# Kernel optimization log

Hardware: AMD Instinct MI355X
Metric: run time of the kernel (lower is better)

The kernel has to match this reference:

```python
import jax, jax.numpy as jnp
import numpy as np

NEG = -1e6  # mask value used by d2l-style masked_softmax


def masked_softmax(scores, valid_lens):
    # scores: [B, Q, K]; valid_lens: [B] int — mask key positions j >= valid_len
    K = scores.shape[-1]
    mask = jnp.arange(K, dtype=jnp.int32)[None, None, :] < valid_lens[:, None, None]
    scores = jnp.where(mask, scores, NEG)
    return jax.nn.softmax(scores, axis=-1)


def setup_inputs() -> dict:
    key = jax.random.key(0)
    kq, kk, kv, kl = jax.random.split(key, 4)
    B, Q, K, d = 16, 4096, 4096, 128
    queries = jax.random.normal(kq, (B, Q, d), dtype=jnp.float32)
    keys = jax.random.normal(kk, (B, K, d), dtype=jnp.float32)
    values = jax.random.normal(kv, (B, K, d), dtype=jnp.float32)
    valid_lens = jax.random.randint(kl, (B,), 1, K + 1, dtype=jnp.int32)
    return {"queries": queries, "keys": keys, "values": values,
            "valid_lens": valid_lens}


def reference(queries, keys, values, valid_lens):
    d = queries.shape[-1]
    # [B, Q, K] scores = Q K^T / sqrt(d)
    scores = jnp.einsum('bqd,bkd->bqk', queries, keys) / jnp.sqrt(
        jnp.asarray(d, queries.dtype))
    attn = masked_softmax(scores, valid_lens)
    # dropout is identity in eval mode
    return jnp.einsum('bqk,bkd->bqd', attn, values)
```

## Files before the change

### kernel.cpp

```cpp
#include <hip/hip_runtime.h>
#include <stdint.h>

typedef __attribute__((ext_vector_type(8))) short short8;
typedef __attribute__((ext_vector_type(4))) float float4v;

#define B_  16
#define S_  4096
#define D_  128
#define TM  64
#define TN  64
#define NT_ (S_ / TN)
#define IMG 8192

__device__ __forceinline__ unsigned short f2bf(float f) {
    union { float f; uint32_t u; } c; c.f = f;
    uint32_t u = c.u + 0x7FFFu + ((c.u >> 16) & 1u);
    return (unsigned short)(u >> 16);
}

__device__ __forceinline__ uint4 pack8(float4v x, float4v y) {
    uint4 r;
    r.x = (uint32_t)f2bf(x[0]) | ((uint32_t)f2bf(x[1]) << 16);
    r.y = (uint32_t)f2bf(x[2]) | ((uint32_t)f2bf(x[3]) << 16);
    r.z = (uint32_t)f2bf(y[0]) | ((uint32_t)f2bf(y[1]) << 16);
    r.w = (uint32_t)f2bf(y[2]) | ((uint32_t)f2bf(y[3]) << 16);
    return r;
}

__device__ __forceinline__ void gload16(const unsigned short* g, unsigned short* l) {
    __builtin_amdgcn_global_load_lds(
        (const __attribute__((address_space(1))) unsigned int*)g,
        (__attribute__((address_space(3))) unsigned int*)l, 16, 0, 0);
}

__global__ __launch_bounds__(256)
void prepass(const float* __restrict__ Kg, const float* __restrict__ Vg,
             unsigned short* __restrict__ Kb, unsigned short* __restrict__ Vb)
{
    const int t = threadIdx.x;
    const int tile = blockIdx.x, b = blockIdx.y;
    const size_t img = (size_t)(b * NT_ + tile) * IMG;

    const float* ksrc = Kg + ((size_t)b * S_ + tile * TN) * D_;
    const float* vsrc = Vg + ((size_t)b * S_ + tile * TN) * D_;
    unsigned short* kdst = Kb + img;
    unsigned short* vdst = Vb + img;

    float4v kx[4], ky[4];
    #pragma unroll
    for (int i = 0; i < 4; ++i) {
        int bid = i * 256 + t;
        int row = bid >> 4, cbp = bid & 15;
        int cb  = cbp ^ (row & 7);
        const float* s = ksrc + row * D_ + cb * 8;
        kx[i] = *(const float4v*)s;
        ky[i] = *(const float4v*)(s + 4);
    }
    const int kb = t >> 5, cg = t & 31;
    float4v v[8];
    #pragma unroll
    for (int r = 0; r < 8; ++r)
        v[r] = *(const float4v*)(vsrc + (kb * 8 + r) * D_ + cg * 4);

    #pragma unroll
    for (int i = 0; i < 4; ++i) {
        int bid = i * 256 + t;
        *(uint4*)(kdst + (size_t)bid * 8) = pack8(kx[i], ky[i]);
    }

    #pragma unroll
    for (int j = 0; j < 4; ++j) {
        int dr = cg * 4 + j;
        uint4 w;
        w.x = (uint32_t)f2bf(v[0][j]) | ((uint32_t)f2bf(v[1][j]) << 16);
        w.y = (uint32_t)f2bf(v[2][j]) | ((uint32_t)f2bf(v[3][j]) << 16);
        w.z = (uint32_t)f2bf(v[4][j]) | ((uint32_t)f2bf(v[5][j]) << 16);
        w.w = (uint32_t)f2bf(v[6][j]) | ((uint32_t)f2bf(v[7][j]) << 16);
        *(uint4*)(vdst + dr * 64 + (kb ^ (dr & 7)) * 8) = w;
    }
}

__global__ __launch_bounds__(256, 4)
void attn_fwd(const float* __restrict__ Qg,
              const unsigned short* __restrict__ Kb,
              const unsigned short* __restrict__ Vb,
              const int* __restrict__ VL,
              float* __restrict__ Og)
{
    __shared__ __align__(16) unsigned short Ks[TN * D_];
    __shared__ __align__(16) unsigned short Vt[D_ * TN];
    __shared__ __align__(16) unsigned short Ps[4 * 16 * 64];

    const int t    = threadIdx.x;
    const int wave = t >> 6;
    const int lane = t & 63;
    const int l16  = lane & 15;
    const int quad = lane >> 4;
    const int sw   = l16 & 7;

    const int b  = blockIdx.y;
    const int q0 = blockIdx.x * TM;
    const int nvalid = VL[b];
    const int ntiles = (nvalid + TN - 1) / TN;

    const float scale = 0.08838834764831845f;

    short8 qf[4];
    {
        const float* qp = Qg + ((size_t)b * S_ + (q0 + wave * 16 + l16)) * D_;
        #pragma unroll
        for (int ks = 0; ks < 4; ++ks) {
            float4v x = *(const float4v*)(qp + ks * 32 + quad * 8);
            float4v y = *(const float4v*)(qp + ks * 32 + quad * 8 + 4);
            #pragma unroll
            for (int j = 0; j < 4; ++j) { x[j] *= scale; y[j] *= scale; }
            union { uint4 u; short8 s; } cv; cv.u = pack8(x, y);
            qf[ks] = cv.s;
        }
    }

    float4v oacc[8];
    #pragma unroll
    for (int dt = 0; dt < 8; ++dt) oacc[dt] = (float4v){0.f, 0.f, 0.f, 0.f};
    float lsum[4] = {0.f, 0.f, 0.f, 0.f};

    unsigned short* Pw = Ps + wave * (16 * 64);

    for (int tile = 0; tile < ntiles; ++tile) {
        const int n0 = tile * TN;
        __syncthreads();

        {
            const unsigned short* kimg = Kb + (size_t)(b * NT_ + tile) * IMG;
            const unsigned short* vimg = Vb + (size_t)(b * NT_ + tile) * IMG;
            #pragma unroll
            for (int i = 0; i < 4; ++i) {
                int go = (i * 256 + t) * 8;
                int lo = (i * 256 + wave * 64) * 8;
                gload16(kimg + go, &Ks[lo]);
                gload16(vimg + go, &Vt[lo]);
            }
        }
        __syncthreads();

        float sv[4][4];
        #pragma unroll
        for (int nt = 0; nt < 4; ++nt) {
            float4v sa = (float4v){0.f, 0.f, 0.f, 0.f};
            #pragma unroll
            for (int ks = 0; ks < 4; ++ks) {
                short8 bf = *(const short8*)(&Ks[(nt * 16 + l16) * D_ + (((ks << 2) + quad) ^ sw) * 8]);
                sa = __builtin_amdgcn_mfma_f32_16x16x32_bf16(qf[ks], bf, sa, 0, 0, 0);
            }
            #pragma unroll
            for (int r = 0; r < 4; ++r) sv[nt][r] = sa[r];
        }

        const bool full = (n0 + TN) <= nvalid;
        #pragma unroll
        for (int nt = 0; nt < 4; ++nt) {
            const bool ok = full || (n0 + nt * 16 + l16) < nvalid;
            const int cb = nt * 2 + (l16 >> 3);
            #pragma unroll
            for (int r = 0; r < 4; ++r) {
                float p = ok ? __expf(sv[nt][r]) : 0.0f;
                lsum[r] += p;
                const int row = quad * 4 + r;
                Pw[row * 64 + ((cb ^ (row >> 1)) << 3) + sw] = f2bf(p);
            }
        }

        #pragma unroll
        for (int ks2 = 0; ks2 < 2; ++ks2) {
            short8 pf = *(const short8*)(&Pw[l16 * 64 + ((((ks2 << 2) + quad) ^ (l16 >> 1)) << 3)]);
            #pragma unroll
            for (int dt = 0; dt < 8; ++dt) {
                short8 vf = *(const short8*)(&Vt[(dt * 16 + l16) * TN + ((((ks2 << 2) + quad) ^ sw) << 3)]);
                oacc[dt] = __builtin_amdgcn_mfma_f32_16x16x32_bf16(pf, vf, oacc[dt], 0, 0, 0);
            }
        }
    }

    float invl[4];
    #pragma unroll
    for (int r = 0; r < 4; ++r) {
        float s = lsum[r];
        #pragma unroll
        for (int off = 1; off < 16; off <<= 1)
            s += __shfl_xor(s, off);
        invl[r] = 1.0f / s;
    }

    float* op = Og + ((size_t)b * S_ + (q0 + wave * 16 + quad * 4)) * D_;
    #pragma unroll
    for (int r = 0; r < 4; ++r) {
        #pragma unroll
        for (int dt = 0; dt < 8; ++dt)
            op[r * D_ + dt * 16 + l16] = oacc[dt][r] * invl[r];
    }
}

extern "C" void kernel_launch(void* const* d_in, const int* in_sizes, int n_in,
                              void* d_out, int out_size, void* d_ws, size_t ws_size,
                              hipStream_t stream) {
    const float* Q = (const float*)d_in[0];
    const float* K = (const float*)d_in[1];
    const float* V = (const float*)d_in[2];
    const int*   L = (const int*)d_in[3];
    float*       O = (float*)d_out;

    unsigned short* Kb = (unsigned short*)d_ws;
    unsigned short* Vb = Kb + (size_t)B_ * S_ * D_;

    dim3 grid(NT_, B_);
    prepass<<<grid, 256, 0, stream>>>(K, V, Kb, Vb);
    dim3 grid2(S_ / TM, B_);
    attn_fwd<<<grid2, 256, 0, stream>>>(Q, Kb, Vb, L, O);
}
```

Before: 227.7 us.

## Switch attention to 32x32 MFMA with transposed S and register-resident P

```diff
diff --git a/kernel.cpp b/kernel.cpp
--- a/kernel.cpp
+++ b/kernel.cpp
@@ -3,6 +3,7 @@
 
 typedef __attribute__((ext_vector_type(8))) short short8;
 typedef __attribute__((ext_vector_type(4))) float float4v;
+typedef __attribute__((ext_vector_type(16))) float f32x16;
 
 #define B_  16
 #define S_  4096
@@ -12,6 +13,8 @@
 #define NT_ (S_ / TN)
 #define IMG 8192
 
+#define ZERO16 {0.f,0.f,0.f,0.f, 0.f,0.f,0.f,0.f, 0.f,0.f,0.f,0.f, 0.f,0.f,0.f,0.f}
+
 __device__ __forceinline__ unsigned short f2bf(float f) {
     union { float f; uint32_t u; } c; c.f = f;
     uint32_t u = c.u + 0x7FFFu + ((c.u >> 16) & 1u);
@@ -33,6 +36,24 @@
         (__attribute__((address_space(3))) unsigned int*)l, 16, 0, 0);
 }
 
+__device__ __forceinline__ uint32_t cvtpk(float lo, float hi) {
+    uint32_t w;
+    asm("v_cvt_pk_bf16_f32 %0, %1, %2" : "=v"(w) : "v"(lo), "v"(hi));
+    return w;
+}
+
+__device__ __forceinline__ short8 build_pfrag(const float* p) {
+    uint32_t xa = cvtpk(p[0], p[1]);
+    uint32_t xb = cvtpk(p[2], p[3]);
+    uint32_t ya = cvtpk(p[4], p[5]);
+    uint32_t yb = cvtpk(p[6], p[7]);
+    asm("v_permlane32_swap_b32 %0, %1" : "+v"(xa), "+v"(ya));
+    asm("v_permlane32_swap_b32 %0, %1" : "+v"(xb), "+v"(yb));
+    union { uint32_t u[4]; short8 s; } r;
+    r.u[0] = xa; r.u[1] = xb; r.u[2] = ya; r.u[3] = yb;
+    return r.s;
+}
+
 __global__ __launch_bounds__(256)
 void prepass(const float* __restrict__ Kg, const float* __restrict__ Vg,
              unsigned short* __restrict__ Kb, unsigned short* __restrict__ Vb)
@@ -51,7 +72,7 @@
     for (int i = 0; i < 4; ++i) {
         int bid = i * 256 + t;
         int row = bid >> 4, cbp = bid & 15;
-        int cb  = cbp ^ (row & 7);
+        int cb  = cbp ^ (row & 15);
         const float* s = ksrc + row * D_ + cb * 8;
         kx[i] = *(const float4v*)s;
         ky[i] = *(const float4v*)(s + 4);
@@ -80,7 +101,7 @@
     }
 }
 
-__global__ __launch_bounds__(256, 4)
+__global__ __launch_bounds__(128, 2)
 void attn_fwd(const float* __restrict__ Qg,
               const unsigned short* __restrict__ Kb,
               const unsigned short* __restrict__ Vb,
@@ -89,42 +110,41 @@
 {
     __shared__ __align__(16) unsigned short Ks[TN * D_];
     __shared__ __align__(16) unsigned short Vt[D_ * TN];
-    __shared__ __align__(16) unsigned short Ps[4 * 16 * 64];
 
     const int t    = threadIdx.x;
     const int wave = t >> 6;
     const int lane = t & 63;
-    const int l16  = lane & 15;
-    const int quad = lane >> 4;
-    const int sw   = l16 & 7;
+    const int l31  = lane & 31;
+    const int hi   = lane >> 5;
 
     const int b  = blockIdx.y;
     const int q0 = blockIdx.x * TM;
     const int nvalid = VL[b];
     const int ntiles = (nvalid + TN - 1) / TN;
 
-    const float scale = 0.08838834764831845f;
-
-    short8 qf[4];
+    const float qscale = 0.08838834764831845f * 1.4426950408889634f;
+
+    short8 qf[8];
     {
-        const float* qp = Qg + ((size_t)b * S_ + (q0 + wave * 16 + l16)) * D_;
+        const float* qp = Qg + ((size_t)b * S_ + (q0 + wave * 32 + l31)) * D_;
         #pragma unroll
-        for (int ks = 0; ks < 4; ++ks) {
-            float4v x = *(const float4v*)(qp + ks * 32 + quad * 8);
-            float4v y = *(const float4v*)(qp + ks * 32 + quad * 8 + 4);
-            #pragma unroll
-            for (int j = 0; j < 4; ++j) { x[j] *= scale; y[j] *= scale; }
+        for (int ks = 0; ks < 8; ++ks) {
+            float4v x = *(const float4v*)(qp + ks * 16 + hi * 8);
+            float4v y = *(const float4v*)(qp + ks * 16 + hi * 8 + 4);
+            #pragma unroll
+            for (int j = 0; j < 4; ++j) { x[j] *= qscale; y[j] *= qscale; }
             union { uint4 u; short8 s; } cv; cv.u = pack8(x, y);
             qf[ks] = cv.s;
         }
     }
 
-    float4v oacc[8];
-    #pragma unroll
-    for (int dt = 0; dt < 8; ++dt) oacc[dt] = (float4v){0.f, 0.f, 0.f, 0.f};
-    float lsum[4] = {0.f, 0.f, 0.f, 0.f};
-
-    unsigned short* Pw = Ps + wave * (16 * 64);
+    f32x16 zz = ZERO16;
+    f32x16 oacc[4];
+    oacc[0] = zz; oacc[1] = zz; oacc[2] = zz; oacc[3] = zz;
+    float lsum = 0.f;
+
+    const int swk = l31 & 15;
+    const int swv = l31 & 7;
 
     for (int tile = 0; tile < ntiles; ++tile) {
         const int n0 = tile * TN;
@@ -134,69 +154,85 @@
             const unsigned short* kimg = Kb + (size_t)(b * NT_ + tile) * IMG;
             const unsigned short* vimg = Vb + (size_t)(b * NT_ + tile) * IMG;
             #pragma unroll
-            for (int i = 0; i < 4; ++i) {
-                int go = (i * 256 + t) * 8;
-                int lo = (i * 256 + wave * 64) * 8;
+            for (int i = 0; i < 8; ++i) {
+                int go = (i * 128 + t) * 8;
+                int lo = (i * 128 + wave * 64) * 8;
                 gload16(kimg + go, &Ks[lo]);
                 gload16(vimg + go, &Vt[lo]);
             }
         }
         __syncthreads();
 
-        float sv[4][4];
+        f32x16 st0 = zz, st1 = zz;
+        {
+            const unsigned short* k0 = &Ks[l31 * D_];
+            const unsigned short* k1 = &Ks[(32 + l31) * D_];
+            __builtin_amdgcn_s_setprio(1);
+            #pragma unroll
+            for (int ks = 0; ks < 8; ++ks) {
+                int sl = (((ks << 1) | hi) ^ swk) << 3;
+                short8 a0 = *(const short8*)(k0 + sl);
+                short8 a1 = *(const short8*)(k1 + sl);
+                st0 = __builtin_amdgcn_mfma_f32_32x32x16_bf16(a0, qf[ks], st0, 0, 0, 0);
+                st1 = __builtin_amdgcn_mfma_f32_32x32x16_bf16(a1, qf[ks], st1, 0, 0, 0);
+            }
+            __builtin_amdgcn_s_setprio(0);
+        }
+
+        float p0[16], p1[16];
+        const bool full = (n0 + TN) <= nvalid;
+        if (full) {
+            #pragma unroll
+            for (int r = 0; r < 16; ++r) { p0[r] = exp2f(st0[r]); lsum += p0[r]; }
+            #pragma unroll
+            for (int r = 0; r < 16; ++r) { p1[r] = exp2f(st1[r]); lsum += p1[r]; }
+        } else {
+            #pragma unroll
+            for (int r = 0; r < 16; ++r) {
+                int key = n0 + (r & 3) + 8 * (r >> 2) + 4 * hi;
+                float e = exp2f(st0[r]);
+                p0[r] = (key < nvalid) ? e : 0.f; lsum += p0[r];
+            }
+            #pragma unroll
+            for (int r = 0; r < 16; ++r) {
+                int key = n0 + 32 + (r & 3) + 8 * (r >> 2) + 4 * hi;
+                float e = exp2f(st1[r]);
+                p1[r] = (key < nvalid) ? e : 0.f; lsum += p1[r];
+            }
+        }
+
+        short8 pf0 = build_pfrag(p0);
+        short8 pf1 = build_pfrag(p0 + 8);
+        short8 pf2 = build_pfrag(p1);
+        short8 pf3 = build_pfrag(p1 + 8);
+
+        __builtin_amdgcn_s_setprio(1);
         #pragma unroll
-        for (int nt = 0; nt < 4; ++nt) {
-            float4v sa = (float4v){0.f, 0.f, 0.f, 0.f};
-            #pragma unroll
-            for (int ks = 0; ks < 4; ++ks) {
-                short8 bf = *(const short8*)(&Ks[(nt * 16 + l16) * D_ + (((ks << 2) + quad) ^ sw) * 8]);
-                sa = __builtin_amdgcn_mfma_f32_16x16x32_bf16(qf[ks], bf, sa, 0, 0, 0);
-            }
-            #pragma unroll
-            for (int r = 0; r < 4; ++r) sv[nt][r] = sa[r];
-        }
-
-        const bool full = (n0 + TN) <= nvalid;
+        for (int dt = 0; dt < 4; ++dt) {
+            const unsigned short* vrow = &Vt[(dt * 32 + l31) * TN];
+            short8 v0 = *(const short8*)(vrow + ((((0 << 1) | hi) ^ swv) << 3));
+            short8 v1 = *(const short8*)(vrow + ((((1 << 1) | hi) ^ swv) << 3));
+            short8 v2 = *(const short8*)(vrow + ((((2 << 1) | hi) ^ swv) << 3));
+            short8 v3 = *(const short8*)(vrow + ((((3 << 1) | hi) ^ swv) << 3));
+            oacc[dt] = __builtin_amdgcn_mfma_f32_32x32x16_bf16(pf0, v0, oacc[dt], 0, 0, 0);
+            oacc[dt] = __builtin_amdgcn_mfma_f32_32x32x16_bf16(pf1, v1, oacc[dt], 0, 0, 0);
+            oacc[dt] = __builtin_amdgcn_mfma_f32_32x32x16_bf16(pf2, v2, oacc[dt], 0, 0, 0);
+            oacc[dt] = __builtin_amdgcn_mfma_f32_32x32x16_bf16(pf3, v3, oacc[dt], 0, 0, 0);
+        }
+        __builtin_amdgcn_s_setprio(0);
+    }
+
+    float ltot = lsum + __shfl_xor(lsum, 32);
+    float inv  = 1.0f / ltot;
+
+    float* op = Og + ((size_t)b * S_ + (q0 + wave * 32)) * D_ + l31;
+    #pragma unroll
+    for (int r = 0; r < 16; ++r) {
+        const int qc = (r & 3) + 8 * (r >> 2);
+        float invr = __shfl(inv, qc + 4 * hi, 32);
         #pragma unroll
-        for (int nt = 0; nt < 4; ++nt) {
-            const bool ok = full || (n0 + nt * 16 + l16) < nvalid;
-            const int cb = nt * 2 + (l16 >> 3);
-            #pragma unroll
-            for (int r = 0; r < 4; ++r) {
-                float p = ok ? __expf(sv[nt][r]) : 0.0f;
-                lsum[r] += p;
-                const int row = quad * 4 + r;
-                Pw[row * 64 + ((cb ^ (row >> 1)) << 3) + sw] = f2bf(p);
-            }
-        }
-
-        #pragma unroll
-        for (int ks2 = 0; ks2 < 2; ++ks2) {
-            short8 pf = *(const short8*)(&Pw[l16 * 64 + ((((ks2 << 2) + quad) ^ (l16 >> 1)) << 3)]);
-            #pragma unroll
-            for (int dt = 0; dt < 8; ++dt) {
-                short8 vf = *(const short8*)(&Vt[(dt * 16 + l16) * TN + ((((ks2 << 2) + quad) ^ sw) << 3)]);
-                oacc[dt] = __builtin_amdgcn_mfma_f32_16x16x32_bf16(pf, vf, oacc[dt], 0, 0, 0);
-            }
-        }
-    }
-
-    float invl[4];
-    #pragma unroll
-    for (int r = 0; r < 4; ++r) {
-        float s = lsum[r];
-        #pragma unroll
-        for (int off = 1; off < 16; off <<= 1)
-            s += __shfl_xor(s, off);
-        invl[r] = 1.0f / s;
-    }
-
-    float* op = Og + ((size_t)b * S_ + (q0 + wave * 16 + quad * 4)) * D_;
-    #pragma unroll
-    for (int r = 0; r < 4; ++r) {
-        #pragma unroll
-        for (int dt = 0; dt < 8; ++dt)
-            op[r * D_ + dt * 16 + l16] = oacc[dt][r] * invl[r];
+        for (int dt = 0; dt < 4; ++dt)
+            op[(qc + 4 * hi) * D_ + dt * 32] = oacc[dt][r] * invr;
     }
 }
 
@@ -215,5 +251,5 @@
     dim3 grid(NT_, B_);
     prepass<<<grid, 256, 0, stream>>>(K, V, Kb, Vb);
     dim3 grid2(S_ / TM, B_);
-    attn_fwd<<<grid2, 256, 0, stream>>>(Q, Kb, Vb, L, O);
-}
+    attn_fwd<<<grid2, 128, 0, stream>>>(Q, Kb, Vb, L, O);
+}
```

New measurement: 240.2 us. 5.5% more time.

## Overlap next K/V tile loads with compute using split waitcnt barriers

Applied to the files above, without the earlier changes.

```diff
diff --git a/kernel.cpp b/kernel.cpp
--- a/kernel.cpp
+++ b/kernel.cpp
@@ -51,7 +51,7 @@
     for (int i = 0; i < 4; ++i) {
         int bid = i * 256 + t;
         int row = bid >> 4, cbp = bid & 15;
-        int cb  = cbp ^ (row & 7);
+        int cb  = cbp ^ (row & 15);
         const float* s = ksrc + row * D_ + cb * 8;
         kx[i] = *(const float4v*)s;
         ky[i] = *(const float4v*)(s + 4);
@@ -96,13 +96,16 @@
     const int lane = t & 63;
     const int l16  = lane & 15;
     const int quad = lane >> 4;
-    const int sw   = l16 & 7;
+    const int swv  = l16 & 7;
 
     const int b  = blockIdx.y;
     const int q0 = blockIdx.x * TM;
     const int nvalid = VL[b];
     const int ntiles = (nvalid + TN - 1) / TN;
 
+    const unsigned short* kbase = Kb + (size_t)b * NT_ * IMG;
+    const unsigned short* vbase = Vb + (size_t)b * NT_ * IMG;
+
     const float scale = 0.08838834764831845f;
 
     short8 qf[4];
@@ -126,22 +129,19 @@
 
     unsigned short* Pw = Ps + wave * (16 * 64);
 
+    #pragma unroll
+    for (int i = 0; i < 4; ++i)
+        gload16(kbase + (i * 256 + t) * 8, &Ks[(i * 256 + wave * 64) * 8]);
+    #pragma unroll
+    for (int i = 0; i < 4; ++i)
+        gload16(vbase + (i * 256 + t) * 8, &Vt[(i * 256 + wave * 64) * 8]);
+
     for (int tile = 0; tile < ntiles; ++tile) {
         const int n0 = tile * TN;
-        __syncthreads();
-
-        {
-            const unsigned short* kimg = Kb + (size_t)(b * NT_ + tile) * IMG;
-            const unsigned short* vimg = Vb + (size_t)(b * NT_ + tile) * IMG;
-            #pragma unroll
-            for (int i = 0; i < 4; ++i) {
-                int go = (i * 256 + t) * 8;
-                int lo = (i * 256 + wave * 64) * 8;
-                gload16(kimg + go, &Ks[lo]);
-                gload16(vimg + go, &Vt[lo]);
-            }
-        }
-        __syncthreads();
+        const int nx = (tile + 1 < ntiles) ? tile + 1 : tile;
+
+        asm volatile("s_waitcnt vmcnt(4)" ::: "memory");
+        __builtin_amdgcn_s_barrier();
 
         float sv[4][4];
         #pragma unroll
@@ -149,11 +149,21 @@
             float4v sa = (float4v){0.f, 0.f, 0.f, 0.f};
             #pragma unroll
             for (int ks = 0; ks < 4; ++ks) {
-                short8 bf = *(const short8*)(&Ks[(nt * 16 + l16) * D_ + (((ks << 2) + quad) ^ sw) * 8]);
+                short8 bf = *(const short8*)(&Ks[(nt * 16 + l16) * D_ + ((((ks << 2) + quad) ^ l16) << 3)]);
                 sa = __builtin_amdgcn_mfma_f32_16x16x32_bf16(qf[ks], bf, sa, 0, 0, 0);
             }
             #pragma unroll
             for (int r = 0; r < 4; ++r) sv[nt][r] = sa[r];
+        }
+
+        asm volatile("s_waitcnt lgkmcnt(0)" ::: "memory");
+        __builtin_amdgcn_s_barrier();
+
+        {
+            const unsigned short* kimg = kbase + (size_t)nx * IMG;
+            #pragma unroll
+            for (int i = 0; i < 4; ++i)
+                gload16(kimg + (i * 256 + t) * 8, &Ks[(i * 256 + wave * 64) * 8]);
         }
 
         const bool full = (n0 + TN) <= nvalid;
@@ -166,20 +176,35 @@
                 float p = ok ? __expf(sv[nt][r]) : 0.0f;
                 lsum[r] += p;
                 const int row = quad * 4 + r;
-                Pw[row * 64 + ((cb ^ (row >> 1)) << 3) + sw] = f2bf(p);
+                Pw[row * 64 + ((cb ^ (row >> 1)) << 3) + swv] = f2bf(p);
             }
         }
+
+        asm volatile("s_waitcnt vmcnt(4)" ::: "memory");
+        __builtin_amdgcn_s_barrier();
 
         #pragma unroll
         for (int ks2 = 0; ks2 < 2; ++ks2) {
             short8 pf = *(const short8*)(&Pw[l16 * 64 + ((((ks2 << 2) + quad) ^ (l16 >> 1)) << 3)]);
             #pragma unroll
             for (int dt = 0; dt < 8; ++dt) {
-                short8 vf = *(const short8*)(&Vt[(dt * 16 + l16) * TN + ((((ks2 << 2) + quad) ^ sw) << 3)]);
+                short8 vf = *(const short8*)(&Vt[(dt * 16 + l16) * TN + ((((ks2 << 2) + quad) ^ swv) << 3)]);
                 oacc[dt] = __builtin_amdgcn_mfma_f32_16x16x32_bf16(pf, vf, oacc[dt], 0, 0, 0);
             }
         }
-    }
+
+        asm volatile("s_waitcnt lgkmcnt(0)" ::: "memory");
+        __builtin_amdgcn_s_barrier();
+
+        {
+            const unsigned short* vimg = vbase + (size_t)nx * IMG;
+            #pragma unroll
+            for (int i = 0; i < 4; ++i)
+                gload16(vimg + (i * 256 + t) * 8, &Vt[(i * 256 + wave * 64) * 8]);
+        }
+    }
+
+    asm volatile("s_waitcnt vmcnt(0)" ::: "memory");
 
     float invl[4];
     #pragma unroll
```

New measurement: 238.5 us. 1.05x slower.

## Fuse K/V bf16 conversion into attention kernel with register prefetch

Applied to the files above, without the earlier changes.

```diff
diff --git a/kernel.cpp b/kernel.cpp
--- a/kernel.cpp
+++ b/kernel.cpp
@@ -10,7 +10,6 @@
 #define TM  64
 #define TN  64
 #define NT_ (S_ / TN)
-#define IMG 8192
 
 __device__ __forceinline__ unsigned short f2bf(float f) {
     union { float f; uint32_t u; } c; c.f = f;
@@ -27,63 +26,10 @@
     return r;
 }
 
-__device__ __forceinline__ void gload16(const unsigned short* g, unsigned short* l) {
-    __builtin_amdgcn_global_load_lds(
-        (const __attribute__((address_space(1))) unsigned int*)g,
-        (__attribute__((address_space(3))) unsigned int*)l, 16, 0, 0);
-}
-
-__global__ __launch_bounds__(256)
-void prepass(const float* __restrict__ Kg, const float* __restrict__ Vg,
-             unsigned short* __restrict__ Kb, unsigned short* __restrict__ Vb)
-{
-    const int t = threadIdx.x;
-    const int tile = blockIdx.x, b = blockIdx.y;
-    const size_t img = (size_t)(b * NT_ + tile) * IMG;
-
-    const float* ksrc = Kg + ((size_t)b * S_ + tile * TN) * D_;
-    const float* vsrc = Vg + ((size_t)b * S_ + tile * TN) * D_;
-    unsigned short* kdst = Kb + img;
-    unsigned short* vdst = Vb + img;
-
-    float4v kx[4], ky[4];
-    #pragma unroll
-    for (int i = 0; i < 4; ++i) {
-        int bid = i * 256 + t;
-        int row = bid >> 4, cbp = bid & 15;
-        int cb  = cbp ^ (row & 7);
-        const float* s = ksrc + row * D_ + cb * 8;
-        kx[i] = *(const float4v*)s;
-        ky[i] = *(const float4v*)(s + 4);
-    }
-    const int kb = t >> 5, cg = t & 31;
-    float4v v[8];
-    #pragma unroll
-    for (int r = 0; r < 8; ++r)
-        v[r] = *(const float4v*)(vsrc + (kb * 8 + r) * D_ + cg * 4);
-
-    #pragma unroll
-    for (int i = 0; i < 4; ++i) {
-        int bid = i * 256 + t;
-        *(uint4*)(kdst + (size_t)bid * 8) = pack8(kx[i], ky[i]);
-    }
-
-    #pragma unroll
-    for (int j = 0; j < 4; ++j) {
-        int dr = cg * 4 + j;
-        uint4 w;
-        w.x = (uint32_t)f2bf(v[0][j]) | ((uint32_t)f2bf(v[1][j]) << 16);
-        w.y = (uint32_t)f2bf(v[2][j]) | ((uint32_t)f2bf(v[3][j]) << 16);
-        w.z = (uint32_t)f2bf(v[4][j]) | ((uint32_t)f2bf(v[5][j]) << 16);
-        w.w = (uint32_t)f2bf(v[6][j]) | ((uint32_t)f2bf(v[7][j]) << 16);
-        *(uint4*)(vdst + dr * 64 + (kb ^ (dr & 7)) * 8) = w;
-    }
-}
-
-__global__ __launch_bounds__(256, 4)
+__global__ __launch_bounds__(256, 3)
 void attn_fwd(const float* __restrict__ Qg,
-              const unsigned short* __restrict__ Kb,
-              const unsigned short* __restrict__ Vb,
+              const float* __restrict__ Kg,
+              const float* __restrict__ Vg,
               const int* __restrict__ VL,
               float* __restrict__ Og)
 {
@@ -96,13 +42,16 @@
     const int lane = t & 63;
     const int l16  = lane & 15;
     const int quad = lane >> 4;
-    const int sw   = l16 & 7;
+    const int swv  = l16 & 7;
 
     const int b  = blockIdx.y;
     const int q0 = blockIdx.x * TM;
     const int nvalid = VL[b];
     const int ntiles = (nvalid + TN - 1) / TN;
 
+    const float* kbase = Kg + (size_t)b * S_ * D_;
+    const float* vbase = Vg + (size_t)b * S_ * D_;
+
     const float scale = 0.08838834764831845f;
 
     short8 qf[4];
@@ -126,22 +75,65 @@
 
     unsigned short* Pw = Ps + wave * (16 * 64);
 
+    const int kb = t >> 5, cg = t & 31;
+
+    float4v kx[4], ky[4], vv[8];
+
+    {
+        const float* ksrc = kbase;
+        #pragma unroll
+        for (int i = 0; i < 4; ++i) {
+            int bid = i * 256 + t;
+            int row = bid >> 4, cb = (bid & 15) ^ (row & 15);
+            const float* s = ksrc + row * D_ + cb * 8;
+            kx[i] = *(const float4v*)s;
+            ky[i] = *(const float4v*)(s + 4);
+        }
+        const float* vsrc = vbase;
+        #pragma unroll
+        for (int r = 0; r < 8; ++r)
+            vv[r] = *(const float4v*)(vsrc + (kb * 8 + r) * D_ + cg * 4);
+    }
+
     for (int tile = 0; tile < ntiles; ++tile) {
         const int n0 = tile * TN;
+        const int nx = (tile + 1 < ntiles) ? tile + 1 : tile;
+
         __syncthreads();
 
+        #pragma unroll
+        for (int i = 0; i < 4; ++i) {
+            int bid = i * 256 + t;
+            *(uint4*)(&Ks[bid * 8]) = pack8(kx[i], ky[i]);
+        }
+        #pragma unroll
+        for (int j = 0; j < 4; ++j) {
+            int dr = cg * 4 + j;
+            uint4 w;
+            w.x = (uint32_t)f2bf(vv[0][j]) | ((uint32_t)f2bf(vv[1][j]) << 16);
+            w.y = (uint32_t)f2bf(vv[2][j]) | ((uint32_t)f2bf(vv[3][j]) << 16);
+            w.z = (uint32_t)f2bf(vv[4][j]) | ((uint32_t)f2bf(vv[5][j]) << 16);
+            w.w = (uint32_t)f2bf(vv[6][j]) | ((uint32_t)f2bf(vv[7][j]) << 16);
+            *(uint4*)(&Vt[dr * 64 + ((kb ^ (dr & 7)) << 3)]) = w;
+        }
+
+        __syncthreads();
+
         {
-            const unsigned short* kimg = Kb + (size_t)(b * NT_ + tile) * IMG;
-            const unsigned short* vimg = Vb + (size_t)(b * NT_ + tile) * IMG;
+            const float* ksrc = kbase + (size_t)nx * TN * D_;
             #pragma unroll
             for (int i = 0; i < 4; ++i) {
-                int go = (i * 256 + t) * 8;
-                int lo = (i * 256 + wave * 64) * 8;
-                gload16(kimg + go, &Ks[lo]);
-                gload16(vimg + go, &Vt[lo]);
-            }
-        }
-        __syncthreads();
+                int bid = i * 256 + t;
+                int row = bid >> 4, cb = (bid & 15) ^ (row & 15);
+                const float* s = ksrc + row * D_ + cb * 8;
+                kx[i] = *(const float4v*)s;
+                ky[i] = *(const float4v*)(s + 4);
+            }
+            const float* vsrc = vbase + (size_t)nx * TN * D_;
+            #pragma unroll
+            for (int r = 0; r < 8; ++r)
+                vv[r] = *(const float4v*)(vsrc + (kb * 8 + r) * D_ + cg * 4);
+        }
 
         float sv[4][4];
         #pragma unroll
@@ -149,7 +141,7 @@
             float4v sa = (float4v){0.f, 0.f, 0.f, 0.f};
             #pragma unroll
             for (int ks = 0; ks < 4; ++ks) {
-                short8 bf = *(const short8*)(&Ks[(nt * 16 + l16) * D_ + (((ks << 2) + quad) ^ sw) * 8]);
+                short8 bf = *(const short8*)(&Ks[(nt * 16 + l16) * D_ + ((((ks << 2) + quad) ^ l16) << 3)]);
                 sa = __builtin_amdgcn_mfma_f32_16x16x32_bf16(qf[ks], bf, sa, 0, 0, 0);
             }
             #pragma unroll
@@ -166,7 +158,7 @@
                 float p = ok ? __expf(sv[nt][r]) : 0.0f;
                 lsum[r] += p;
                 const int row = quad * 4 + r;
-                Pw[row * 64 + ((cb ^ (row >> 1)) << 3) + sw] = f2bf(p);
+                Pw[row * 64 + ((cb ^ (row >> 1)) << 3) + swv] = f2bf(p);
             }
         }
 
@@ -175,7 +167,7 @@
             short8 pf = *(const short8*)(&Pw[l16 * 64 + ((((ks2 << 2) + quad) ^ (l16 >> 1)) << 3)]);
             #pragma unroll
             for (int dt = 0; dt < 8; ++dt) {
-                short8 vf = *(const short8*)(&Vt[(dt * 16 + l16) * TN + ((((ks2 << 2) + quad) ^ sw) << 3)]);
+                short8 vf = *(const short8*)(&Vt[(dt * 16 + l16) * TN + ((((ks2 << 2) + quad) ^ swv) << 3)]);
                 oacc[dt] = __builtin_amdgcn_mfma_f32_16x16x32_bf16(pf, vf, oacc[dt], 0, 0, 0);
             }
         }
@@ -209,11 +201,6 @@
     const int*   L = (const int*)d_in[3];
     float*       O = (float*)d_out;
 
-    unsigned short* Kb = (unsigned short*)d_ws;
-    unsigned short* Vb = Kb + (size_t)B_ * S_ * D_;
-
-    dim3 grid(NT_, B_);
-    prepass<<<grid, 256, 0, stream>>>(K, V, Kb, Vb);
-    dim3 grid2(S_ / TM, B_);
-    attn_fwd<<<grid2, 256, 0, stream>>>(Q, Kb, Vb, L, O);
-}
+    dim3 grid(S_ / TM, B_);
+    attn_fwd<<<grid, 256, 0, stream>>>(Q, K, V, L, O);
+}
```

Result: slower. 330.0 us (+44.9%).
